# Kernel optimization log

Measured on AMD Instinct MI355X. Metric: run time of the kernel, lower is better.

Reference implementation:

```python
import jax, jax.numpy as jnp
import numpy as np

HEADS = 8


def setup_inputs() -> dict:
    key = jax.random.key(0)
    k1, k2, k3, k4, k5 = jax.random.split(key, 5)
    bt, b_sz, n, dim = 2, 4, 1024, 512
    inner6 = 3072  # inner_dim * 6 where inner_dim = heads * dim_head = 512
    return {
        "x": jax.random.normal(k1, (bt, b_sz, n, dim), dtype=jnp.float32),
        "W_qkv": jax.random.normal(k2, (dim, inner6), dtype=jnp.float32) * 0.02,
        "b_qkv": jax.random.normal(k3, (inner6,), dtype=jnp.float32) * 0.02,
        "W_out": jax.random.normal(k4, (1024, dim), dtype=jnp.float32) * 0.02,
        "b_out": jax.random.normal(k5, (dim,), dtype=jnp.float32) * 0.02,
    }


def reference(x, W_qkv, b_qkv, W_out, b_out):
    bt, b_sz, n, dim = x.shape
    # to_qkv: Linear(dim, 3072) -> reshape (bt,b,n,3,H,hd) -> transpose(2,4)
    qkv = (x @ W_qkv + b_qkv).reshape(bt, b_sz, n, 3, HEADS, -1)
    qkv = qkv.transpose(0, 1, 4, 3, 2, 5)  # (bt, b, H, 3, n, hd)
    q, k, v = qkv[:, :, :, 0], qkv[:, :, :, 1], qkv[:, :, :, 2]
    scale = (dim // HEADS) ** -0.5  # faithful: uses dim//heads, not per-head width
    attn = jax.nn.softmax(jnp.einsum("abhnd,abhmd->abhnm", q * scale, k), axis=-1)
    out = jnp.einsum("abhnm,abhmd->abhnd", attn, v)
    out = out.transpose(0, 1, 3, 2, 4).reshape(bt, b_sz, n, -1)  # (bt,b,n,H*hd)
    return out @ W_out + b_out
```

## Files before the change

### kernel.cpp

```cpp
#include <hip/hip_runtime.h>

typedef __attribute__((ext_vector_type(4))) float f32x4;
typedef __attribute__((ext_vector_type(16))) float f32x16;
typedef __attribute__((ext_vector_type(8))) __bf16 bf16x8;
typedef __attribute__((ext_vector_type(8))) unsigned short ushortx8;
typedef unsigned short u16;
typedef unsigned int u32;

#define AS1 __attribute__((address_space(1)))
#define AS3 __attribute__((address_space(3)))

__device__ __forceinline__ void gld_lds16(const void* g, void* s) {
  __builtin_amdgcn_global_load_lds((AS1 void*)g, (AS3 void*)s, 16, 0, 0);
}

__device__ __forceinline__ u16 f2bf(float f) {
  unsigned int u = __float_as_uint(f);
  unsigned int r = (u + 0x7FFFu + ((u >> 16) & 1u)) >> 16;
  return (u16)r;
}

#define QSCALE 0.1803368801111244f

__global__ void cvt_f32_bf16(const float* __restrict__ src, u16* __restrict__ dst, int n) {
  int i = (blockIdx.x * blockDim.x + threadIdx.x) * 8;
  if (i >= n) return;
  const float4 a = *(const float4*)&src[i];
  const float4 b = *(const float4*)&src[i + 4];
  ushortx8 o;
  o[0] = f2bf(a.x); o[1] = f2bf(a.y); o[2] = f2bf(a.z); o[3] = f2bf(a.w);
  o[4] = f2bf(b.x); o[5] = f2bf(b.y); o[6] = f2bf(b.z); o[7] = f2bf(b.w);
  *(ushortx8*)&dst[i] = o;
}

__global__ void scale_bias(const float* __restrict__ src, float* __restrict__ dst, int n,
                           int boundary, float s) {
  int i = blockIdx.x * blockDim.x + threadIdx.x;
  if (i < n) dst[i] = src[i] * (i < boundary ? s : 1.0f);
}

__global__ void transpose_to_bf16(const float* __restrict__ src, u16* __restrict__ dst,
                                  int R, int C, int boundary, float s) {
  __shared__ float tile[32][33];
  const int c0 = blockIdx.x * 32, r0 = blockIdx.y * 32;
  const int tx = threadIdx.x, ty = threadIdx.y;
  #pragma unroll
  for (int i = ty; i < 32; i += 8)
    tile[i][tx] = src[(size_t)(r0 + i) * C + c0 + tx];
  __syncthreads();
  #pragma unroll
  for (int i = ty; i < 32; i += 8) {
    const float sc = (c0 + i < boundary) ? s : 1.0f;
    dst[(size_t)(c0 + i) * R + r0 + tx] = f2bf(tile[tx][i] * sc);
  }
}

__global__ void transpose_v(const u16* __restrict__ qkv, u16* __restrict__ vt) {
  __shared__ u16 tile[32][34];
  const int bh = blockIdx.z, b = bh >> 3, h = bh & 7;
  const int n0 = blockIdx.y * 32, d0 = blockIdx.x * 32;
  const int tx = threadIdx.x, ty = threadIdx.y;
  const u16* src = qkv + (size_t)(b * 1024) * 3072 + 2048 + h * 128;
  #pragma unroll
  for (int i = ty; i < 32; i += 8)
    tile[i][tx] = src[(size_t)(n0 + i) * 3072 + d0 + tx];
  __syncthreads();
  u16* dst = vt + (size_t)(b * 8 + h) * 128 * 1024;
  #pragma unroll
  for (int i = ty; i < 32; i += 8)
    dst[(size_t)(d0 + i) * 1024 + n0 + tx] = tile[tx][i];
}

template <int BM, int BN, int BK, int OUT_BF16>
__global__ __launch_bounds__(256, 4) void gemm_bt(const u16* __restrict__ A,
                                                  const u16* __restrict__ Bt,
                                                  const float* __restrict__ bias,
                                                  void* __restrict__ Cv,
                                                  int M, int N, int K) {
  constexpr int RPC = 512 / BK;
  constexpr int LPR = BK / 8;
  constexpr int MASK = LPR - 1;
  constexpr int P = 64 / BK > 0 ? 64 / BK : 1;
  constexpr int CA = BM / RPC, CB = BN / RPC;
  constexpr int CAW = CA / 4, CBW = CB / 4;
  constexpr int VM = CAW + CBW;
  constexpr int FM = BM / 32, FN = BN / 32;
  constexpr int KS = BK / 32;

  __shared__ __attribute__((aligned(16))) u16 As[2][BM * BK];
  __shared__ __attribute__((aligned(16))) u16 Bs[2][BN * BK];
  const int nwg = gridDim.x * gridDim.y;
  int bid = blockIdx.y * gridDim.x + blockIdx.x;
  if ((nwg & 7) == 0) bid = (bid & 7) * (nwg >> 3) + (bid >> 3);
  const int n0 = (bid % gridDim.x) * BN, m0 = (bid / gridDim.x) * BM;
  const int tid = threadIdx.x;
  const int w = tid >> 6, l = tid & 63;
  const int wr = w >> 1, wc = w & 1;
  const int lr = l >> 4, lc = l & 15;
  f32x4 acc[FM][FN] = {};

#define GSTAGE(bi, k0)                                                          \
  do {                                                                          \
    _Pragma("unroll") for (int i = 0; i < CAW; ++i) {                           \
      const int c = w * CAW + i;                                                \
      const int row = c * RPC + l / LPR;                                        \
      const int col = ((l % LPR) ^ ((row / P) & MASK)) * 8;                     \
      gld_lds16(&A[(size_t)(m0 + row) * K + (k0) + col], &As[bi][c * 512]);     \
    }                                                                           \
    _Pragma("unroll") for (int i = 0; i < CBW; ++i) {                           \
      const int c = w * CBW + i;                                                \
      const int row = c * RPC + l / LPR;                                        \
      const int col = ((l % LPR) ^ ((row / P) & MASK)) * 8;                     \
      gld_lds16(&Bt[(size_t)(n0 + row) * K + (k0) + col], &Bs[bi][c * 512]);    \
    }                                                                           \
  } while (0)

#define GCOMP(bi)                                                                      \
  do {                                                                                 \
    _Pragma("unroll") for (int ks = 0; ks < KS; ++ks) {                                \
      bf16x8 af[FM], bfr[FN];                                                          \
      _Pragma("unroll") for (int m = 0; m < FM; ++m) {                                 \
        const int row = wr * (BM / 2) + m * 16 + lc;                                   \
        af[m] = *(const bf16x8*)&As[bi][row * BK +                                     \
                                        (((ks * 4 + lr) ^ ((row / P) & MASK)) << 3)];  \
      }                                                                                \
      _Pragma("unroll") for (int n = 0; n < FN; ++n) {                                 \
        const int row = wc * (BN / 2) + n * 16 + lc;                                   \
        bfr[n] = *(const bf16x8*)&Bs[bi][row * BK +                                    \
                                         (((ks * 4 + lr) ^ ((row / P) & MASK)) << 3)]; \
      }                                                                                \
      __builtin_amdgcn_s_setprio(1);                                                   \
      _Pragma("unroll") for (int m = 0; m < FM; ++m)                                   \
          _Pragma("unroll") for (int n = 0; n < FN; ++n)                               \
              acc[m][n] =                                                              \
          __builtin_amdgcn_mfma_f32_16x16x32_bf16(af[m], bfr[n], acc[m][n], 0, 0, 0);  \
      __builtin_amdgcn_s_setprio(0);                                                   \
    }                                                                                  \
  } while (0)

  GSTAGE(0, 0);
  int buf = 0;
  for (int k0 = BK; k0 < K; k0 += BK) {
    GSTAGE(buf ^ 1, k0);
    if constexpr (VM == 4)
      asm volatile("s_waitcnt vmcnt(4)" ::: "memory");
    else if constexpr (VM == 2)
      asm volatile("s_waitcnt vmcnt(2)" ::: "memory");
    else
      asm volatile("s_waitcnt vmcnt(8)" ::: "memory");
    __builtin_amdgcn_s_barrier();
    __builtin_amdgcn_sched_barrier(0);
    GCOMP(buf);
    __builtin_amdgcn_s_barrier();
    buf ^= 1;
  }
  asm volatile("s_waitcnt vmcnt(0)" ::: "memory");
  __builtin_amdgcn_s_barrier();
  __builtin_amdgcn_sched_barrier(0);
  GCOMP(buf);
#undef GSTAGE
#undef GCOMP

  #pragma unroll
  for (int n = 0; n < FN; ++n) {
    const int col = n0 + wc * (BN / 2) + n * 16 + lc;
    const float bv = bias[col];
    #pragma unroll
    for (int m = 0; m < FM; ++m) {
      #pragma unroll
      for (int r = 0; r < 4; ++r) {
        const int row = m0 + wr * (BM / 2) + m * 16 + lr * 4 + r;
        const float v = acc[m][n][r] + bv;
        if (OUT_BF16)
          ((u16*)Cv)[(size_t)row * N + col] = f2bf(v);
        else
          ((float*)Cv)[(size_t)row * N + col] = v;
      }
    }
  }
}

__global__ __launch_bounds__(512, 2) void gemm_qkv_8ph(const u16* __restrict__ A,
                                                       const u16* __restrict__ Bt,
                                                       const float* __restrict__ bias,
                                                       u16* __restrict__ C,
                                                       int M, int N, int K) {
  __shared__ __attribute__((aligned(16))) u16 As[2][256 * 64];
  __shared__ __attribute__((aligned(16))) u16 Bs[2][192 * 64];
  const int nwg = gridDim.x;
  int bid = blockIdx.x;
  if ((nwg & 7) == 0) bid = (bid & 7) * (nwg >> 3) + (bid >> 3);
  const int ntile = N / 192;
  const int n0 = (bid % ntile) * 192, m0 = (bid / ntile) * 256;
  const int tid = threadIdx.x;
  const int w = tid >> 6, l = tid & 63;
  const int wr = w >> 2, wc = w & 3;
  const int lr = l >> 4, lc = l & 15;
  f32x4 acc[8][3] = {};
  bf16x8 af[2][2], bfv[3][2];

#define STAGE_A(bi, kt, h)                                                          \
  do {                                                                              \
    _Pragma("unroll") for (int cc = 0; cc < 2; ++cc) {                              \
      const int cib = (h) * 1024 + (cc * 8 + w) * 64;                               \
      const int ci = cib + l;                                                       \
      const int row = ci >> 3, ck = ci & 7;                                         \
      gld_lds16(&A[(size_t)(m0 + row) * K + (kt) * 64 + ((ck ^ (row & 7)) << 3)],   \
                &As[bi][cib * 8]);                                                  \
    }                                                                               \
  } while (0)

#define STAGE_B(bi, kt, t)                                                          \
  do {                                                                              \
    const int cib = (t) * 512 + w * 64;                                             \
    const int ci = cib + l;                                                         \
    const int row = ci >> 3, ck = ci & 7;                                           \
    gld_lds16(&Bt[(size_t)(n0 + row) * K + (kt) * 64 + ((ck ^ (row & 7)) << 3)],    \
              &Bs[bi][cib * 8]);                                                    \
  } while (0)

#define RD_A(bi, mp)                                                                \
  do {                                                                              \
    _Pragma("unroll") for (int m2 = 0; m2 < 2; ++m2)                                \
      _Pragma("unroll") for (int ks = 0; ks < 2; ++ks) {                            \
        const int row = wr * 128 + (2 * (mp) + m2) * 16 + lc;                       \
        af[m2][ks] = *(const bf16x8*)&As[bi][row * 64 +                             \
                                             (((ks * 4 + lr) ^ (lc & 7)) << 3)];    \
      }                                                                             \
  } while (0)

#define RD_B(bi)                                                                    \
  do {                                                                              \
    _Pragma("unroll") for (int n = 0; n < 3; ++n)                                   \
      _Pragma("unroll") for (int ks = 0; ks < 2; ++ks) {                            \
        const int row = wc * 48 + n * 16 + lc;                                      \
        bfv[n][ks] = *(const bf16x8*)&Bs[bi][row * 64 +                             \
                                             (((ks * 4 + lr) ^ (lc & 7)) << 3)];    \
      }                                                                             \
  } while (0)

#define MM(mp)                                                                      \
  do {                                                                              \
    __builtin_amdgcn_s_setprio(1);                                                  \
    _Pragma("unroll") for (int m2 = 0; m2 < 2; ++m2)                                \
      _Pragma("unroll") for (int n = 0; n < 3; ++n)                                 \
        _Pragma("unroll") for (int ks = 0; ks < 2; ++ks)                            \
          acc[2 * (mp) + m2][n] = __builtin_amdgcn_mfma_f32_16x16x32_bf16(          \
              af[m2][ks], bfv[n][ks], acc[2 * (mp) + m2][n], 0, 0, 0);              \
    __builtin_amdgcn_s_setprio(0);                                                  \
  } while (0)

#define BARC()                                                                      \
  do {                                                                              \
    __builtin_amdgcn_s_barrier();                                                   \
    asm volatile("s_waitcnt lgkmcnt(0)" ::: "memory");                              \
    __builtin_amdgcn_sched_barrier(0);                                              \
  } while (0)

  STAGE_B(0, 0, 0); STAGE_B(0, 0, 1); STAGE_B(0, 0, 2);
  STAGE_A(0, 0, 0); STAGE_A(0, 0, 1);
  STAGE_B(1, 1, 0); STAGE_B(1, 1, 1);
  asm volatile("s_waitcnt vmcnt(2)" ::: "memory");
  __builtin_amdgcn_s_barrier();
  __builtin_amdgcn_sched_barrier(0);

  const int NI = K >> 7;
  for (int i = 0; i < NI; ++i) {
    const bool nl = (i < NI - 1);
    const int tO = 2 * i + 1, tE2 = 2 * i + 2, tO2 = 2 * i + 3;
    RD_B(0); RD_A(0, 0);
    STAGE_B(1, tO, 2); STAGE_A(1, tO, 0); STAGE_A(1, tO, 1);
    BARC(); MM(0);
    __builtin_amdgcn_s_barrier();
    RD_A(0, 1);
    if (nl) STAGE_B(0, tE2, 0);
    BARC(); MM(1);
    __builtin_amdgcn_s_barrier();
    RD_A(0, 2);
    if (nl) STAGE_B(0, tE2, 1);
    BARC(); MM(2);
    __builtin_amdgcn_s_barrier();
    RD_A(0, 3);
    if (nl) STAGE_B(0, tE2, 2);
    BARC(); MM(3);
    if (nl) asm volatile("s_waitcnt vmcnt(3)" ::: "memory");
    else    asm volatile("s_waitcnt vmcnt(0)" ::: "memory");
    __builtin_amdgcn_s_barrier();
    __builtin_amdgcn_sched_barrier(0);
    RD_B(1); RD_A(1, 0);
    if (nl) STAGE_A(0, tE2, 0);
    BARC(); MM(0);
    __builtin_amdgcn_s_barrier();
    RD_A(1, 1);
    if (nl) STAGE_A(0, tE2, 1);
    BARC(); MM(1);
    __builtin_amdgcn_s_barrier();
    RD_A(1, 2);
    if (nl) STAGE_B(1, tO2, 0);
    BARC(); MM(2);
    __builtin_amdgcn_s_barrier();
    RD_A(1, 3);
    if (nl) STAGE_B(1, tO2, 1);
    BARC(); MM(3);
    if (nl) {
      asm volatile("s_waitcnt vmcnt(2)" ::: "memory");
      __builtin_amdgcn_s_barrier();
      __builtin_amdgcn_sched_barrier(0);
    }
  }
#undef STAGE_A
#undef STAGE_B
#undef RD_A
#undef RD_B
#undef MM
#undef BARC

  #pragma unroll
  for (int n = 0; n < 3; ++n) {
    const int col = n0 + wc * 48 + n * 16 + lc;
    const float bv = bias[col];
    #pragma unroll
    for (int m = 0; m < 8; ++m) {
      #pragma unroll
      for (int r = 0; r < 4; ++r) {
        const int row = m0 + wr * 128 + m * 16 + lr * 4 + r;
        C[(size_t)row * N + col] = f2bf(acc[m][n][r] + bv);
      }
    }
  }
}

__global__ __launch_bounds__(256, 2) void attn_fwd(const u16* __restrict__ qkv,
                                                   const u16* __restrict__ vt,
                                                   u16* __restrict__ attn_out) {
  __shared__ __attribute__((aligned(16))) u16 Ks[2][64 * 128];
  __shared__ __attribute__((aligned(16))) u16 Vs[2][64 * 128];
  const int orig = blockIdx.y * 8 + blockIdx.x;
  const int swz = (orig & 7) * 64 + (orig >> 3);
  const int bh = swz >> 3, b = bh >> 3, h = bh & 7;
  const int q0 = (swz & 7) * 128;
  const int tid = threadIdx.x, w = tid >> 6, l = tid & 63;
  const int ll = l & 31, hi = l >> 5;
  const int wq0 = q0 + w * 32;
  const u16* Qb = qkv + (size_t)(b * 1024 + wq0) * 3072 + h * 128;
  const u16* Kb = qkv + (size_t)(b * 1024) * 3072 + 1024 + h * 128;
  const u16* Vb = vt + (size_t)(b * 8 + h) * 128 * 1024;

  bf16x8 bq[8];
  #pragma unroll
  for (int s = 0; s < 8; ++s)
    bq[s] = *(const bf16x8*)&Qb[(size_t)ll * 3072 + s * 16 + hi * 8];
  asm volatile("s_waitcnt vmcnt(0)" ::: "memory");

  bf16x8 ones;
  #pragma unroll
  for (int i = 0; i < 8; ++i) ones[i] = (__bf16)1.0f;

  const u16* sb[8];
  int dst0;
  if (w < 2) {
    #pragma unroll
    for (int j = 0; j < 8; ++j) {
      const int r = w * 32 + j * 4 + (l >> 4);
      const int c = l & 15;
      sb[j] = Kb + (size_t)r * 3072 + ((c ^ (r & 15)) << 3);
    }
    dst0 = w * 4096;
  } else {
    #pragma unroll
    for (int j = 0; j < 8; ++j) {
      const int r2 = (w - 2) * 32 + j * 4 + (l >> 4);
      const int c = l & 15;
      const int d = ((c >> 3) ^ ((r2 >> 3) & 1)) * 64 + (r2 >> 5) * 32 + (r2 & 31);
      const int kc = (c & 7) ^ (r2 & 7);
      sb[j] = Vb + (size_t)d * 1024 + (kc << 3);
    }
    dst0 = (w - 2) * 4096;
  }

#define STAGE(bi, tt)                                                            \
  do {                                                                           \
    if (w < 2) {                                                                 \
      _Pragma("unroll") for (int j = 0; j < 8; ++j)                              \
          gld_lds16(sb[j] + (size_t)(tt)*196608, &Ks[bi][dst0 + j * 512]);       \
    } else {                                                                     \
      _Pragma("unroll") for (int j = 0; j < 8; ++j)                              \
          gld_lds16(sb[j] + (size_t)(tt)*64, &Vs[bi][dst0 + j * 512]);           \
    }                                                                            \
  } while (0)

#define QK(Kt)                                                                     \
  do {                                                                            \
    st0 = (f32x16){};                                                             \
    st1 = (f32x16){};                                                             \
    __builtin_amdgcn_s_setprio(1);                                                \
    _Pragma("unroll") for (int s = 0; s < 8; ++s) {                               \
      const int ch = ((s * 2 + hi) ^ (ll & 15)) << 3;                             \
      const bf16x8 ak0 = *(const bf16x8*)&(Kt)[ll * 128 + ch];                    \
      const bf16x8 ak1 = *(const bf16x8*)&(Kt)[(32 + ll) * 128 + ch];             \
      st0 = __builtin_amdgcn_mfma_f32_32x32x16_bf16(ak0, bq[s], st0, 0, 0, 0);    \
      st1 = __builtin_amdgcn_mfma_f32_32x32x16_bf16(ak1, bq[s], st1, 0, 0, 0);    \
    }                                                                             \
    __builtin_amdgcn_s_setprio(0);                                                \
  } while (0)

#define SOFTMAX()                                                                  \
  do {                                                                            \
    _Pragma("unroll") for (int kb = 0; kb < 2; ++kb) {                            \
      float pe[16];                                                               \
      _Pragma("unroll") for (int r = 0; r < 16; ++r)                              \
          pe[r] = exp2f(kb ? st1[r] : st0[r]);                                    \
      _Pragma("unroll") for (int j = 0; j < 8; ++j) {                             \
        u32 d_;                                                                   \
        asm("v_cvt_pk_bf16_f32 %0, %1, %2"                                        \
            : "=v"(d_)                                                            \
            : "v"(pe[2 * j]), "v"(pe[2 * j + 1]));                                \
        mm[kb * 8 + j] = d_;                                                      \
      }                                                                           \
      asm volatile("v_permlane32_swap_b32 %0, %1"                                 \
                   : "+v"(mm[kb * 8 + 0]), "+v"(mm[kb * 8 + 2]));                 \
      asm volatile("v_permlane32_swap_b32 %0, %1"                                 \
                   : "+v"(mm[kb * 8 + 1]), "+v"(mm[kb * 8 + 3]));                 \
      asm volatile("v_permlane32_swap_b32 %0, %1"                                 \
                   : "+v"(mm[kb * 8 + 4]), "+v"(mm[kb * 8 + 6]));                 \
      asm volatile("v_permlane32_swap_b32 %0, %1"                                 \
                   : "+v"(mm[kb * 8 + 5]), "+v"(mm[kb * 8 + 7]));                 \
    }                                                                             \
  } while (0)

#define PV(Vt_)                                                                    \
  do {                                                                            \
    __builtin_amdgcn_s_setprio(1);                                                \
    _Pragma("unroll") for (int kb = 0; kb < 2; ++kb) {                            \
      _Pragma("unroll") for (int s2 = 0; s2 < 2; ++s2) {                          \
        union { u32 u[4]; bf16x8 v; } pu;                                         \
        pu.u[0] = mm[kb * 8 + s2 * 4 + 0];                                        \
        pu.u[1] = mm[kb * 8 + s2 * 4 + 1];                                        \
        pu.u[2] = mm[kb * 8 + s2 * 4 + 2];                                        \
        pu.u[3] = mm[kb * 8 + s2 * 4 + 3];                                        \
        const bf16x8 pa = pu.v;                                                   \
        acc_l = __builtin_amdgcn_mfma_f32_32x32x16_bf16(pa, ones, acc_l, 0, 0, 0);\
        _Pragma("unroll") for (int db = 0; db < 4; ++db) {                        \
          const int r2 = (db & 1) * 32 + ll;                                      \
          const int c = ((((db >> 1) ^ ((ll >> 3) & 1)) << 3) |                   \
                         ((kb * 4 + s2 * 2 + hi) ^ (ll & 7)));                    \
          const bf16x8 bv = *(const bf16x8*)&(Vt_)[r2 * 128 + c * 8];             \
          acc_o[db] =                                                             \
              __builtin_amdgcn_mfma_f32_32x32x16_bf16(pa, bv, acc_o[db], 0, 0, 0);\
        }                                                                         \
      }                                                                           \
    }                                                                             \
    __builtin_amdgcn_s_setprio(0);                                                \
  } while (0)

  f32x16 acc_o[4] = {};
  f32x16 acc_l = {};
  f32x16 st0, st1;
  u32 mm[16];

  STAGE(0, 0);
  int buf = 0;
  for (int t = 0; t < 15; ++t) {
    STAGE(buf ^ 1, t + 1);
    asm volatile("s_waitcnt vmcnt(8)" ::: "memory");
    __builtin_amdgcn_s_barrier();
    __builtin_amdgcn_sched_barrier(0);
    QK(Ks[buf]);
    SOFTMAX();
    PV(Vs[buf]);
    __builtin_amdgcn_s_barrier();
    buf ^= 1;
  }
  asm volatile("s_waitcnt vmcnt(0)" ::: "memory");
  __builtin_amdgcn_s_barrier();
  __builtin_amdgcn_sched_barrier(0);
  QK(Ks[buf]);
  SOFTMAX();
  PV(Vs[buf]);

#undef STAGE
#undef QK
#undef SOFTMAX
#undef PV

  float inv[16];
  #pragma unroll
  for (int r = 0; r < 16; ++r) inv[r] = __builtin_amdgcn_rcpf(acc_l[r]);
  u16* Ob = attn_out + (size_t)(b * 1024 + wq0) * 1024 + h * 128;
  #pragma unroll
  for (int db = 0; db < 4; ++db)
    #pragma unroll
    for (int r = 0; r < 16; ++r) {
      const int q = (r & 3) + 8 * (r >> 2) + 4 * hi;
      Ob[(size_t)q * 1024 + db * 32 + ll] = f2bf(acc_o[db][r] * inv[r]);
    }
}

extern "C" void kernel_launch(void* const* d_in, const int* in_sizes, int n_in,
                              void* d_out, int out_size, void* d_ws, size_t ws_size,
                              hipStream_t stream) {
  const float* x = (const float*)d_in[0];
  const float* Wqkv = (const float*)d_in[1];
  const float* bqkv = (const float*)d_in[2];
  const float* Wout = (const float*)d_in[3];
  const float* bout = (const float*)d_in[4];
  float* out = (float*)d_out;

  char* ws = (char*)d_ws;
  u16* xb    = (u16*)(ws);
  u16* wqkvt = (u16*)(ws + 8388608);
  u16* woutt = (u16*)(ws + 8388608 + 3145728);
  u16* qkvb  = (u16*)(ws + 12582912);
  u16* vtb   = (u16*)(ws + 62914560);
  u16* aob   = (u16*)(ws + 79691776);
  float* bq2 = (float*)aob;

  cvt_f32_bf16<<<2048, 256, 0, stream>>>(x, xb, 8192 * 512);
  scale_bias<<<12, 256, 0, stream>>>(bqkv, bq2, 3072, 1024, QSCALE);
  transpose_to_bf16<<<dim3(96, 16), dim3(32, 8), 0, stream>>>(Wqkv, wqkvt, 512, 3072, 1024, QSCALE);
  transpose_to_bf16<<<dim3(16, 32), dim3(32, 8), 0, stream>>>(Wout, woutt, 1024, 512, 0, 1.0f);

  gemm_qkv_8ph<<<dim3(512), 512, 0, stream>>>(xb, wqkvt, bq2, qkvb, 8192, 3072, 512);

  transpose_v<<<dim3(4, 32, 64), dim3(32, 8), 0, stream>>>(qkvb, vtb);

  attn_fwd<<<dim3(8, 64), 256, 0, stream>>>(qkvb, vtb, aob);

  gemm_bt<64, 64, 32, 0><<<dim3(8, 128), 256, 0, stream>>>(aob, woutt, bout, out,
                                                           8192, 512, 1024);
}
```

Baseline: 133.6 us.

## Software-pipeline attention QK/PV across tiles and stage QKV GEMM epilogue through LDS

The attention loop is restructured so that QK for tile t is issued alongside PV for tile t-1, with a triple-buffered V tile in shared memory. This lets matrix-core work overlap with the softmax dependency chain. Separately, the QKV GEMM epilogue now writes results into shared memory and then stores 16-byte coalesced rows, replacing scattered 2-byte global stores. The costs are extra LDS use (a third V buffer) and additional barriers, and PV now reads its softmax probabilities one iteration late, which raises register pressure.

New measurement: 132.2 us. Within noise of the previous version (-1.1%).

```diff
diff --git a/kernel.cpp b/kernel.cpp
--- a/kernel.cpp
+++ b/kernel.cpp
@@ -185,8 +185,9 @@
                                                        const float* __restrict__ bias,
                                                        u16* __restrict__ C,
                                                        int M, int N, int K) {
-  __shared__ __attribute__((aligned(16))) u16 As[2][256 * 64];
-  __shared__ __attribute__((aligned(16))) u16 Bs[2][192 * 64];
+  __shared__ __attribute__((aligned(16))) u16 SMEM[57344];
+  u16* const AsP[2] = {SMEM, SMEM + 16384};
+  u16* const BsP[2] = {SMEM + 32768, SMEM + 45056};
   const int nwg = gridDim.x;
   int bid = blockIdx.x;
   if ((nwg & 7) == 0) bid = (bid & 7) * (nwg >> 3) + (bid >> 3);
@@ -206,7 +207,7 @@
       const int ci = cib + l;                                                       \
       const int row = ci >> 3, ck = ci & 7;                                         \
       gld_lds16(&A[(size_t)(m0 + row) * K + (kt) * 64 + ((ck ^ (row & 7)) << 3)],   \
-                &As[bi][cib * 8]);                                                  \
+                &AsP[bi][cib * 8]);                                                 \
     }                                                                               \
   } while (0)
 
@@ -216,7 +217,7 @@
     const int ci = cib + l;                                                         \
     const int row = ci >> 3, ck = ci & 7;                                           \
     gld_lds16(&Bt[(size_t)(n0 + row) * K + (kt) * 64 + ((ck ^ (row & 7)) << 3)],    \
-              &Bs[bi][cib * 8]);                                                    \
+              &BsP[bi][cib * 8]);                                                   \
   } while (0)
 
 #define RD_A(bi, mp)                                                                \
@@ -224,8 +225,8 @@
     _Pragma("unroll") for (int m2 = 0; m2 < 2; ++m2)                                \
       _Pragma("unroll") for (int ks = 0; ks < 2; ++ks) {                            \
         const int row = wr * 128 + (2 * (mp) + m2) * 16 + lc;                       \
-        af[m2][ks] = *(const bf16x8*)&As[bi][row * 64 +                             \
-                                             (((ks * 4 + lr) ^ (lc & 7)) << 3)];    \
+        af[m2][ks] = *(const bf16x8*)&AsP[bi][row * 64 +                            \
+                                              (((ks * 4 + lr) ^ (lc & 7)) << 3)];   \
       }                                                                             \
   } while (0)
 
@@ -234,8 +235,8 @@
     _Pragma("unroll") for (int n = 0; n < 3; ++n)                                   \
       _Pragma("unroll") for (int ks = 0; ks < 2; ++ks) {                            \
         const int row = wc * 48 + n * 16 + lc;                                      \
-        bfv[n][ks] = *(const bf16x8*)&Bs[bi][row * 64 +                             \
-                                             (((ks * 4 + lr) ^ (lc & 7)) << 3)];    \
+        bfv[n][ks] = *(const bf16x8*)&BsP[bi][row * 64 +                            \
+                                              (((ks * 4 + lr) ^ (lc & 7)) << 3)];   \
       }                                                                             \
   } while (0)
 
@@ -315,18 +316,26 @@
 #undef MM
 #undef BARC
 
+  __builtin_amdgcn_s_barrier();
   #pragma unroll
   for (int n = 0; n < 3; ++n) {
-    const int col = n0 + wc * 48 + n * 16 + lc;
-    const float bv = bias[col];
+    const float bv = bias[n0 + wc * 48 + n * 16 + lc];
     #pragma unroll
     for (int m = 0; m < 8; ++m) {
       #pragma unroll
       for (int r = 0; r < 4; ++r) {
-        const int row = m0 + wr * 128 + m * 16 + lr * 4 + r;
-        C[(size_t)row * N + col] = f2bf(acc[m][n][r] + bv);
+        const int row = wr * 128 + m * 16 + lr * 4 + r;
+        SMEM[row * 192 + wc * 48 + n * 16 + lc] = f2bf(acc[m][n][r] + bv);
       }
     }
+  }
+  __builtin_amdgcn_s_barrier();
+  #pragma unroll
+  for (int it = 0; it < 12; ++it) {
+    const int chunk = it * 512 + tid;
+    const int row = chunk / 24, c16 = chunk % 24;
+    const bf16x8 v = *(const bf16x8*)&SMEM[row * 192 + c16 * 8];
+    *(bf16x8*)&C[(size_t)(m0 + row) * N + n0 + c16 * 8] = v;
   }
 }
 
@@ -334,7 +343,7 @@
                                                    const u16* __restrict__ vt,
                                                    u16* __restrict__ attn_out) {
   __shared__ __attribute__((aligned(16))) u16 Ks[2][64 * 128];
-  __shared__ __attribute__((aligned(16))) u16 Vs[2][64 * 128];
+  __shared__ __attribute__((aligned(16))) u16 Vs[3][64 * 128];
   const int orig = blockIdx.y * 8 + blockIdx.x;
   const int swz = (orig & 7) * 64 + (orig >> 3);
   const int bh = swz >> 3, b = bh >> 3, h = bh & 7;
@@ -378,14 +387,14 @@
     dst0 = (w - 2) * 4096;
   }
 
-#define STAGE(bi, tt)                                                            \
+#define STAGE(ki, vi, tt)                                                        \
   do {                                                                           \
     if (w < 2) {                                                                 \
       _Pragma("unroll") for (int j = 0; j < 8; ++j)                              \
-          gld_lds16(sb[j] + (size_t)(tt)*196608, &Ks[bi][dst0 + j * 512]);       \
+          gld_lds16(sb[j] + (size_t)(tt)*196608, &Ks[ki][dst0 + j * 512]);       \
     } else {                                                                     \
       _Pragma("unroll") for (int j = 0; j < 8; ++j)                              \
-          gld_lds16(sb[j] + (size_t)(tt)*64, &Vs[bi][dst0 + j * 512]);           \
+          gld_lds16(sb[j] + (size_t)(tt)*64, &Vs[vi][dst0 + j * 512]);           \
     }                                                                            \
   } while (0)
 
@@ -458,25 +467,27 @@
   f32x16 st0, st1;
   u32 mm[16];
 
-  STAGE(0, 0);
-  int buf = 0;
-  for (int t = 0; t < 15; ++t) {
-    STAGE(buf ^ 1, t + 1);
-    asm volatile("s_waitcnt vmcnt(8)" ::: "memory");
-    __builtin_amdgcn_s_barrier();
-    __builtin_amdgcn_sched_barrier(0);
-    QK(Ks[buf]);
-    SOFTMAX();
-    PV(Vs[buf]);
-    __builtin_amdgcn_s_barrier();
-    buf ^= 1;
-  }
-  asm volatile("s_waitcnt vmcnt(0)" ::: "memory");
+  STAGE(0, 0, 0);
+  STAGE(1, 1, 1);
+  asm volatile("s_waitcnt vmcnt(8)" ::: "memory");
   __builtin_amdgcn_s_barrier();
   __builtin_amdgcn_sched_barrier(0);
-  QK(Ks[buf]);
+  QK(Ks[0]);
   SOFTMAX();
-  PV(Vs[buf]);
+  __builtin_amdgcn_s_barrier();
+
+  for (int t = 1; t < 16; ++t) {
+    if (t < 15) STAGE((t + 1) & 1, (t + 1) % 3, t + 1);
+    if (t < 15) asm volatile("s_waitcnt vmcnt(8)" ::: "memory");
+    else        asm volatile("s_waitcnt vmcnt(0)" ::: "memory");
+    __builtin_amdgcn_s_barrier();
+    __builtin_amdgcn_sched_barrier(0);
+    QK(Ks[t & 1]);
+    PV(Vs[(t - 1) % 3]);
+    SOFTMAX();
+    __builtin_amdgcn_s_barrier();
+  }
+  PV(Vs[0]);
 
 #undef STAGE
 #undef QK
```

## Coarsen QKV GEMM phases and stage epilogue through LDS for vector stores

Applied to the files above, without the earlier changes.

Restructures the QKV GEMM main loop from eight sub-phases per iteration into four. Each phase now reads twice as many A fragments and issues its B or A tile loads in larger batches, which halves the number of barriers. The epilogue now writes bias-added bf16 results into LDS, which reuses the staging buffers as one flat array, and then emits coalesced 16-byte global stores instead of scattered 2-byte stores. This costs more VGPRs for the doubled A fragments and adds two barriers plus an LDS round trip in the epilogue.

Result: no change. 132.6 us (-0.8%).

```diff
diff --git a/kernel.cpp b/kernel.cpp
--- a/kernel.cpp
+++ b/kernel.cpp
@@ -185,8 +185,9 @@
                                                        const float* __restrict__ bias,
                                                        u16* __restrict__ C,
                                                        int M, int N, int K) {
-  __shared__ __attribute__((aligned(16))) u16 As[2][256 * 64];
-  __shared__ __attribute__((aligned(16))) u16 Bs[2][192 * 64];
+  __shared__ __attribute__((aligned(16))) u16 SMEM[57344];
+  u16* const AsP[2] = {SMEM, SMEM + 16384};
+  u16* const BsP[2] = {SMEM + 32768, SMEM + 45056};
   const int nwg = gridDim.x;
   int bid = blockIdx.x;
   if ((nwg & 7) == 0) bid = (bid & 7) * (nwg >> 3) + (bid >> 3);
@@ -197,7 +198,7 @@
   const int wr = w >> 2, wc = w & 3;
   const int lr = l >> 4, lc = l & 15;
   f32x4 acc[8][3] = {};
-  bf16x8 af[2][2], bfv[3][2];
+  bf16x8 af[2][2][2], bfv[3][2];
 
 #define STAGE_A(bi, kt, h)                                                          \
   do {                                                                              \
@@ -206,7 +207,7 @@
       const int ci = cib + l;                                                       \
       const int row = ci >> 3, ck = ci & 7;                                         \
       gld_lds16(&A[(size_t)(m0 + row) * K + (kt) * 64 + ((ck ^ (row & 7)) << 3)],   \
-                &As[bi][cib * 8]);                                                  \
+                &AsP[bi][cib * 8]);                                                 \
     }                                                                               \
   } while (0)
 
@@ -216,17 +217,18 @@
     const int ci = cib + l;                                                         \
     const int row = ci >> 3, ck = ci & 7;                                           \
     gld_lds16(&Bt[(size_t)(n0 + row) * K + (kt) * 64 + ((ck ^ (row & 7)) << 3)],    \
-              &Bs[bi][cib * 8]);                                                    \
-  } while (0)
-
-#define RD_A(bi, mp)                                                                \
+              &BsP[bi][cib * 8]);                                                   \
+  } while (0)
+
+#define RD_A2(bi, hf)                                                               \
   do {                                                                              \
-    _Pragma("unroll") for (int m2 = 0; m2 < 2; ++m2)                                \
-      _Pragma("unroll") for (int ks = 0; ks < 2; ++ks) {                            \
-        const int row = wr * 128 + (2 * (mp) + m2) * 16 + lc;                       \
-        af[m2][ks] = *(const bf16x8*)&As[bi][row * 64 +                             \
-                                             (((ks * 4 + lr) ^ (lc & 7)) << 3)];    \
-      }                                                                             \
+    _Pragma("unroll") for (int q = 0; q < 2; ++q)                                   \
+      _Pragma("unroll") for (int m2 = 0; m2 < 2; ++m2)                              \
+        _Pragma("unroll") for (int ks = 0; ks < 2; ++ks) {                          \
+          const int row = wr * 128 + ((hf) * 4 + q * 2 + m2) * 16 + lc;             \
+          af[q][m2][ks] = *(const bf16x8*)&AsP[bi][row * 64 +                       \
+                                                   (((ks * 4 + lr) ^ (lc & 7)) << 3)]; \
+        }                                                                           \
   } while (0)
 
 #define RD_B(bi)                                                                    \
@@ -234,19 +236,20 @@
     _Pragma("unroll") for (int n = 0; n < 3; ++n)                                   \
       _Pragma("unroll") for (int ks = 0; ks < 2; ++ks) {                            \
         const int row = wc * 48 + n * 16 + lc;                                      \
-        bfv[n][ks] = *(const bf16x8*)&Bs[bi][row * 64 +                             \
-                                             (((ks * 4 + lr) ^ (lc & 7)) << 3)];    \
+        bfv[n][ks] = *(const bf16x8*)&BsP[bi][row * 64 +                            \
+                                              (((ks * 4 + lr) ^ (lc & 7)) << 3)];   \
       }                                                                             \
   } while (0)
 
-#define MM(mp)                                                                      \
+#define MM2(hf)                                                                     \
   do {                                                                              \
     __builtin_amdgcn_s_setprio(1);                                                  \
-    _Pragma("unroll") for (int m2 = 0; m2 < 2; ++m2)                                \
-      _Pragma("unroll") for (int n = 0; n < 3; ++n)                                 \
-        _Pragma("unroll") for (int ks = 0; ks < 2; ++ks)                            \
-          acc[2 * (mp) + m2][n] = __builtin_amdgcn_mfma_f32_16x16x32_bf16(          \
-              af[m2][ks], bfv[n][ks], acc[2 * (mp) + m2][n], 0, 0, 0);              \
+    _Pragma("unroll") for (int q = 0; q < 2; ++q)                                   \
+      _Pragma("unroll") for (int m2 = 0; m2 < 2; ++m2)                              \
+        _Pragma("unroll") for (int n = 0; n < 3; ++n)                               \
+          _Pragma("unroll") for (int ks = 0; ks < 2; ++ks)                          \
+            acc[(hf) * 4 + q * 2 + m2][n] = __builtin_amdgcn_mfma_f32_16x16x32_bf16(\
+                af[q][m2][ks], bfv[n][ks], acc[(hf) * 4 + q * 2 + m2][n], 0, 0, 0); \
     __builtin_amdgcn_s_setprio(0);                                                  \
   } while (0)
 
@@ -259,8 +262,8 @@
 
   STAGE_B(0, 0, 0); STAGE_B(0, 0, 1); STAGE_B(0, 0, 2);
   STAGE_A(0, 0, 0); STAGE_A(0, 0, 1);
-  STAGE_B(1, 1, 0); STAGE_B(1, 1, 1);
-  asm volatile("s_waitcnt vmcnt(2)" ::: "memory");
+  STAGE_B(1, 1, 0); STAGE_B(1, 1, 1); STAGE_B(1, 1, 2);
+  asm volatile("s_waitcnt vmcnt(3)" ::: "memory");
   __builtin_amdgcn_s_barrier();
   __builtin_amdgcn_sched_barrier(0);
 
@@ -268,65 +271,57 @@
   for (int i = 0; i < NI; ++i) {
     const bool nl = (i < NI - 1);
     const int tO = 2 * i + 1, tE2 = 2 * i + 2, tO2 = 2 * i + 3;
-    RD_B(0); RD_A(0, 0);
-    STAGE_B(1, tO, 2); STAGE_A(1, tO, 0); STAGE_A(1, tO, 1);
-    BARC(); MM(0);
-    __builtin_amdgcn_s_barrier();
-    RD_A(0, 1);
-    if (nl) STAGE_B(0, tE2, 0);
-    BARC(); MM(1);
-    __builtin_amdgcn_s_barrier();
-    RD_A(0, 2);
-    if (nl) STAGE_B(0, tE2, 1);
-    BARC(); MM(2);
-    __builtin_amdgcn_s_barrier();
-    RD_A(0, 3);
-    if (nl) STAGE_B(0, tE2, 2);
-    BARC(); MM(3);
+    RD_B(0); RD_A2(0, 0);
+    STAGE_A(1, tO, 0); STAGE_A(1, tO, 1);
+    BARC(); MM2(0);
+    __builtin_amdgcn_s_barrier();
+    RD_A2(0, 1);
+    if (nl) { STAGE_B(0, tE2, 0); STAGE_B(0, tE2, 1); STAGE_B(0, tE2, 2); }
+    BARC(); MM2(1);
     if (nl) asm volatile("s_waitcnt vmcnt(3)" ::: "memory");
     else    asm volatile("s_waitcnt vmcnt(0)" ::: "memory");
     __builtin_amdgcn_s_barrier();
     __builtin_amdgcn_sched_barrier(0);
-    RD_B(1); RD_A(1, 0);
-    if (nl) STAGE_A(0, tE2, 0);
-    BARC(); MM(0);
-    __builtin_amdgcn_s_barrier();
-    RD_A(1, 1);
-    if (nl) STAGE_A(0, tE2, 1);
-    BARC(); MM(1);
-    __builtin_amdgcn_s_barrier();
-    RD_A(1, 2);
-    if (nl) STAGE_B(1, tO2, 0);
-    BARC(); MM(2);
-    __builtin_amdgcn_s_barrier();
-    RD_A(1, 3);
-    if (nl) STAGE_B(1, tO2, 1);
-    BARC(); MM(3);
+    RD_B(1); RD_A2(1, 0);
+    if (nl) { STAGE_A(0, tE2, 0); STAGE_A(0, tE2, 1); }
+    BARC(); MM2(0);
+    __builtin_amdgcn_s_barrier();
+    RD_A2(1, 1);
+    if (nl) { STAGE_B(1, tO2, 0); STAGE_B(1, tO2, 1); STAGE_B(1, tO2, 2); }
+    BARC(); MM2(1);
     if (nl) {
-      asm volatile("s_waitcnt vmcnt(2)" ::: "memory");
+      asm volatile("s_waitcnt vmcnt(3)" ::: "memory");
       __builtin_amdgcn_s_barrier();
       __builtin_amdgcn_sched_barrier(0);
     }
   }
 #undef STAGE_A
 #undef STAGE_B
-#undef RD_A
+#undef RD_A2
 #undef RD_B
-#undef MM
+#undef MM2
 #undef BARC
 
+  __builtin_amdgcn_s_barrier();
   #pragma unroll
   for (int n = 0; n < 3; ++n) {
-    const int col = n0 + wc * 48 + n * 16 + lc;
-    const float bv = bias[col];
+    const float bv = bias[n0 + wc * 48 + n * 16 + lc];
     #pragma unroll
     for (int m = 0; m < 8; ++m) {
       #pragma unroll
       for (int r = 0; r < 4; ++r) {
-        const int row = m0 + wr * 128 + m * 16 + lr * 4 + r;
-        C[(size_t)row * N + col] = f2bf(acc[m][n][r] + bv);
+        const int row = wr * 128 + m * 16 + lr * 4 + r;
+        SMEM[row * 192 + wc * 48 + n * 16 + lc] = f2bf(acc[m][n][r] + bv);
       }
     }
+  }
+  __builtin_amdgcn_s_barrier();
+  #pragma unroll
+  for (int it = 0; it < 12; ++it) {
+    const int chunk = it * 512 + tid;
+    const int row = chunk / 24, c16 = chunk % 24;
+    const bf16x8 v = *(const bf16x8*)&SMEM[row * 192 + c16 * 8];
+    *(bf16x8*)&C[(size_t)(m0 + row) * N + n0 + c16 * 8] = v;
   }
 }
 
```
